# Optimization experiments

Measured on AMD Instinct MI355X. Metric: run time of the kernel, lower is better.

The kernel has to match this reference:

```python
import jax, jax.numpy as jnp
import numpy as np

B, C, H, W, K = 16, 256, 64, 64, 31
PAD = K // 2
EPS = 1e-5


def setup_inputs() -> dict:
    key = jax.random.key(0)
    k1, k2, k3 = jax.random.split(key, 3)
    x = jax.random.normal(k1, (B, C, H, W), dtype=jnp.float32)
    dw_w = jax.random.normal(k2, (C, 1, K, K), dtype=jnp.float32) * 0.02
    pw_w = jax.random.normal(k3, (C, C), dtype=jnp.float32) * 0.05
    gamma = jnp.ones((C,), dtype=jnp.float32)
    beta = jnp.zeros((C,), dtype=jnp.float32)
    return {"x": x, "dw_w": dw_w, "gamma": gamma, "beta": beta, "pw_w": pw_w}


def reference(x, dw_w, gamma, beta, pw_w):
    # depthwise 31x31 conv, padding=15, groups=C
    y = jax.lax.conv_general_dilated(
        x, dw_w,
        window_strides=(1, 1),
        padding=[(PAD, PAD), (PAD, PAD)],
        dimension_numbers=("NCHW", "OIHW", "NCHW"),
        feature_group_count=C,
    )
    # BatchNorm2d in training mode: biased batch stats over (N,H,W)
    mean = jnp.mean(y, axis=(0, 2, 3), keepdims=True)
    var = jnp.var(y, axis=(0, 2, 3), keepdims=True)  # biased, as torch uses for normalization
    g = gamma[None, :, None, None]
    b = beta[None, :, None, None]
    yn = (y - mean) * jax.lax.rsqrt(var + EPS) * g + b
    r = jax.nn.relu(yn)
    # pointwise 1x1 conv == channel-mixing matmul
    out = jnp.einsum("oc,bchw->bohw", pw_w, r)
    return out
```

## Files before the change

### kernel.cpp

```cpp
#include <hip/hip_runtime.h>
#include <hip/hip_bf16.h>

namespace {
constexpr int CB   = 256;
constexpr int HWp  = 4096;
constexpr int NB   = 16;

typedef __bf16    bf16x8 __attribute__((ext_vector_type(8)));
typedef float     f32x4  __attribute__((ext_vector_type(4)));
typedef float     f32x16 __attribute__((ext_vector_type(16)));
typedef _Float16  f16x2  __attribute__((ext_vector_type(2)));
typedef _Float16  f16x8  __attribute__((ext_vector_type(8)));

typedef __attribute__((address_space(1))) void gvoid;
typedef __attribute__((address_space(3))) void svoid;

__device__ __forceinline__ unsigned int pack2(float lo, float hi) {
#if __has_builtin(__builtin_amdgcn_cvt_pkrtz)
    return __builtin_bit_cast(unsigned int, __builtin_amdgcn_cvt_pkrtz(lo, hi));
#else
    f16x2 v; v[0] = (_Float16)lo; v[1] = (_Float16)hi;
    return __builtin_bit_cast(unsigned int, v);
#endif
}

constexpr int TOEP_PER_C = 31 * 4 * 64;
}

__global__ __launch_bounds__(256) void toep_kernel(
    const float* __restrict__ dw, uint4* __restrict__ toep)
{
    const int flat = blockIdx.x * 256 + threadIdx.x;
    const int lane = flat & 63;
    const int kq   = (flat >> 6) & 3;
    const int rc   = flat >> 8;
    const int r    = rc % 31;
    const int c    = rc / 31;
    const int i    = lane & 31;
    const int kbase = kq * 16 + (lane >> 5) * 8;

    const float* __restrict__ wr = dw + (size_t)c * 961 + r * 31;
    union { _Float16 h[8]; uint4 u; } out;
#pragma unroll
    for (int e = 0; e < 8; ++e) {
        const int t = kbase + e - i - 1;
        out.h[e] = (t >= 0 && t <= 30) ? (_Float16)wr[t] : (_Float16)0.f;
    }
    toep[flat] = out.u;
}

__global__ __launch_bounds__(256, 5) void dwconv_kernel(
    const float* __restrict__ x, const uint4* __restrict__ toep,
    float* __restrict__ y, float* __restrict__ gsum, float* __restrict__ gsumsq)
{
    __shared__ unsigned int xs[94 * 52];

    const int bc  = blockIdx.x;
    const int c   = bc & (CB - 1);
    const int tid = threadIdx.x;
    const float* __restrict__ xp = x + (size_t)bc * HWp;

    for (int idx = tid; idx < 1222; idx += 256)
        reinterpret_cast<uint4*>(xs)[idx] = uint4{0, 0, 0, 0};
    __syncthreads();
    {
        const int row = tid >> 2;
        const int q   = tid & 3;
        const float4* src = reinterpret_cast<const float4*>(xp + row * 64 + q * 16);
        float4 v0 = src[0], v1 = src[1], v2 = src[2], v3 = src[3];
        uint4 p0, p1;
        p0.x = pack2(v0.x, v0.y); p0.y = pack2(v0.z, v0.w);
        p0.z = pack2(v1.x, v1.y); p0.w = pack2(v1.z, v1.w);
        p1.x = pack2(v2.x, v2.y); p1.y = pack2(v2.z, v2.w);
        p1.z = pack2(v3.x, v3.y); p1.w = pack2(v3.z, v3.w);
        uint4* dst = reinterpret_cast<uint4*>(&xs[(row + 15) * 52 + 8 + q * 8]);
        dst[0] = p0; dst[1] = p1;
    }
    __syncthreads();

    const int lane = tid & 63;
    const int wid  = tid >> 6;
    const int h0   = wid * 16;
    const int j    = lane & 31;
    const int half = lane >> 5;

    const unsigned int* __restrict__ xb =
        &xs[(h0 + (j >> 1)) * 52 + (j & 1) * 16 + half * 4];
    const uint4* __restrict__ tp = toep + (size_t)c * TOEP_PER_C + lane;

    f32x16 acc = {};

    uint4 afA[4]; f16x8 bfA[4];
#pragma unroll
    for (int kq = 0; kq < 4; ++kq) {
        afA[kq] = tp[kq * 64];
        bfA[kq] = *reinterpret_cast<const f16x8*>(xb + kq * 8);
    }
#pragma unroll 2
    for (int r = 0; r < 31; ++r) {
        uint4 afB[4]; f16x8 bfB[4];
        if (r < 30) {
            const unsigned int* xr = xb + (r + 1) * 52;
#pragma unroll
            for (int kq = 0; kq < 4; ++kq) {
                afB[kq] = tp[((r + 1) * 4 + kq) * 64];
                bfB[kq] = *reinterpret_cast<const f16x8*>(xr + kq * 8);
            }
        }
#pragma unroll
        for (int kq = 0; kq < 4; ++kq)
            acc = __builtin_amdgcn_mfma_f32_32x32x16_f16(
                __builtin_bit_cast(f16x8, afA[kq]), bfA[kq], acc, 0, 0, 0);
#pragma unroll
        for (int kq = 0; kq < 4; ++kq) { afA[kq] = afB[kq]; bfA[kq] = bfB[kq]; }
    }

    const int hout = h0 + (j >> 1);
    float* __restrict__ yp = y + (size_t)bc * HWp + hout * 64 + (j & 1) * 32 + 4 * half;
#pragma unroll
    for (int g = 0; g < 4; ++g) {
        f32x4 v = { acc[4 * g + 0], acc[4 * g + 1], acc[4 * g + 2], acc[4 * g + 3] };
        *reinterpret_cast<f32x4*>(yp + 8 * g) = v;
    }

    float s = 0.f, s2 = 0.f;
#pragma unroll
    for (int t = 0; t < 16; ++t) { s += acc[t]; s2 = fmaf(acc[t], acc[t], s2); }
#pragma unroll
    for (int off = 32; off > 0; off >>= 1) {
        s  += __shfl_down(s,  off, 64);
        s2 += __shfl_down(s2, off, 64);
    }
    if (lane == 0) {
        atomicAdd(&gsum[c],   s);
        atomicAdd(&gsumsq[c], s2);
    }
}

__global__ __launch_bounds__(256) void pwb_kernel(
    const float* __restrict__ pw, __hip_bfloat16* __restrict__ pwb)
{
    const int idx = blockIdx.x * 256 + threadIdx.x;
    const float4 v = reinterpret_cast<const float4*>(pw)[idx];
    union { __hip_bfloat16 h[4]; uint2 u; } pk;
    pk.h[0] = __float2bfloat16(v.x); pk.h[1] = __float2bfloat16(v.y);
    pk.h[2] = __float2bfloat16(v.z); pk.h[3] = __float2bfloat16(v.w);
    reinterpret_cast<uint2*>(pwb)[idx] = pk.u;
}

__global__ __launch_bounds__(256) void stats_kernel(
    const float* __restrict__ gsum, const float* __restrict__ gsumsq,
    const float* __restrict__ gamma, const float* __restrict__ beta,
    float* __restrict__ scale, float* __restrict__ shift)
{
    const int tid = threadIdx.x;
    const float inv = 1.f / 65536.f;
    const float mean = gsum[tid] * inv;
    const float var  = gsumsq[tid] * inv - mean * mean;
    const float sc   = gamma[tid] * rsqrtf(var + 1e-5f);
    scale[tid] = sc;
    shift[tid] = beta[tid] - mean * sc;
}

__global__ __launch_bounds__(256) void normtrans_kernel(
    const float* __restrict__ y, const float* __restrict__ scale,
    const float* __restrict__ shift, __hip_bfloat16* __restrict__ rt)
{
    __shared__ __hip_bfloat16 tile[32][33];
    const int b   = blockIdx.z;
    const int c0  = blockIdx.y * 32;
    const int p0  = blockIdx.x * 32;
    const int tid = threadIdx.x;

    {
        const int cl  = tid >> 3;
        const int pl4 = (tid & 7) * 4;
        const float4 v = *reinterpret_cast<const float4*>(
            y + (size_t)(b * CB + c0 + cl) * HWp + p0 + pl4);
        const float sc = scale[c0 + cl], sh = shift[c0 + cl];
        tile[cl][pl4 + 0] = __float2bfloat16(fmaxf(fmaf(v.x, sc, sh), 0.f));
        tile[cl][pl4 + 1] = __float2bfloat16(fmaxf(fmaf(v.y, sc, sh), 0.f));
        tile[cl][pl4 + 2] = __float2bfloat16(fmaxf(fmaf(v.z, sc, sh), 0.f));
        tile[cl][pl4 + 3] = __float2bfloat16(fmaxf(fmaf(v.w, sc, sh), 0.f));
    }
    __syncthreads();
    {
        const int pl  = tid >> 3;
        const int cl4 = (tid & 7) * 4;
        union { __hip_bfloat16 h[4]; uint2 u; } pk;
#pragma unroll
        for (int k2 = 0; k2 < 4; ++k2) pk.h[k2] = tile[cl4 + k2][pl];
        *reinterpret_cast<uint2*>(
            rt + ((size_t)b * HWp + p0 + pl) * CB + c0 + cl4) = pk.u;
    }
}

__global__ __launch_bounds__(256, 2) void gemm_kernel(
    const __hip_bfloat16* __restrict__ pwb, const __hip_bfloat16* __restrict__ rt,
    float* __restrict__ out)
{
    __shared__ __hip_bfloat16 ldsA[128 * 32];
    __shared__ __hip_bfloat16 ldsB[128 * 32];

    const int tid  = threadIdx.x;
    const int lane = tid & 63;
    const int wid  = tid >> 6;
    const int b    = blockIdx.z;
    const int m0   = blockIdx.y * 128;
    const int p0   = blockIdx.x * 128;
    const int wm   = wid >> 1, wn = wid & 1;

    f32x4 acc[4][4];
#pragma unroll
    for (int mi = 0; mi < 4; ++mi)
#pragma unroll
        for (int ni = 0; ni < 4; ++ni) acc[mi][ni] = {0.f, 0.f, 0.f, 0.f};

    const int srow = lane >> 2;
    const int scol = (lane & 3) * 8;
    const int fr   = lane & 15;
    const int fk   = (lane >> 4) * 8;

    const size_t rtbase = (size_t)b * HWp;

    for (int ks = 0; ks < 8; ++ks) {
        const int k0 = ks * 32;
#pragma unroll
        for (int q = 0; q < 2; ++q) {
            const int issue = wid * 2 + q;
            const int row   = issue * 16 + srow;
            const __hip_bfloat16* gA = pwb + (size_t)(m0 + row) * CB + k0 + scol;
            const __hip_bfloat16* gB = rt + (rtbase + p0 + row) * CB + k0 + scol;
            __builtin_amdgcn_global_load_lds((gvoid*)gA, (svoid*)(ldsA + issue * 512), 16, 0, 0);
            __builtin_amdgcn_global_load_lds((gvoid*)gB, (svoid*)(ldsB + issue * 512), 16, 0, 0);
        }
        __syncthreads();

        bf16x8 af[4], bfr[4];
#pragma unroll
        for (int mi = 0; mi < 4; ++mi)
            af[mi] = *reinterpret_cast<const bf16x8*>(
                ldsA + (wm * 64 + mi * 16 + fr) * 32 + fk);
#pragma unroll
        for (int ni = 0; ni < 4; ++ni)
            bfr[ni] = *reinterpret_cast<const bf16x8*>(
                ldsB + (wn * 64 + ni * 16 + fr) * 32 + fk);

#pragma unroll
        for (int mi = 0; mi < 4; ++mi)
#pragma unroll
            for (int ni = 0; ni < 4; ++ni)
                acc[mi][ni] = __builtin_amdgcn_mfma_f32_16x16x32_bf16(
                    af[mi], bfr[ni], acc[mi][ni], 0, 0, 0);
        __syncthreads();
    }

    const int frow = (lane >> 4) * 4;
#pragma unroll
    for (int mi = 0; mi < 4; ++mi)
#pragma unroll
        for (int ni = 0; ni < 4; ++ni)
#pragma unroll
            for (int v = 0; v < 4; ++v) {
                const int o = m0 + wm * 64 + mi * 16 + frow + v;
                const int p = p0 + wn * 64 + ni * 16 + fr;
                out[((size_t)(b * CB + o)) * HWp + p] = acc[mi][ni][v];
            }
}

extern "C" void kernel_launch(void* const* d_in, const int* in_sizes, int n_in,
                              void* d_out, int out_size, void* d_ws, size_t ws_size,
                              hipStream_t stream) {
    (void)in_sizes; (void)n_in; (void)out_size; (void)ws_size;
    const float* x     = (const float*)d_in[0];
    const float* dw    = (const float*)d_in[1];
    const float* gamma = (const float*)d_in[2];
    const float* beta  = (const float*)d_in[3];
    const float* pw    = (const float*)d_in[4];
    float* out = (float*)d_out;

    char* ws = (char*)d_ws;
    uint4* toep        = (uint4*)ws;
    __hip_bfloat16* rt = (__hip_bfloat16*)ws;
    float* gsum   = (float*)(ws + (size_t)33554432);
    float* gsumsq = gsum + 256;
    float* scale  = gsum + 512;
    float* shift  = gsum + 768;
    __hip_bfloat16* pwb = (__hip_bfloat16*)(ws + (size_t)33554432 + 4096);

    hipMemsetAsync(gsum, 0, 2048, stream);

    pwb_kernel<<<dim3(64), 256, 0, stream>>>(pw, pwb);
    toep_kernel<<<dim3(7936), 256, 0, stream>>>(dw, toep);
    dwconv_kernel<<<dim3(NB * CB), 256, 0, stream>>>(x, toep, out, gsum, gsumsq);
    stats_kernel<<<dim3(1), 256, 0, stream>>>(gsum, gsumsq, gamma, beta, scale, shift);
    normtrans_kernel<<<dim3(128, 8, NB), 256, 0, stream>>>(out, scale, shift, rt);
    gemm_kernel<<<dim3(32, 2, NB), 256, 0, stream>>>(pwb, rt, out);
}
```

Before: 243.6 us.

## Process two images per dwconv block, store fp16 intermediate, fuse small prep kernels

The depthwise conv block now handles two batch images of the same channel, so each Toeplitz weight fragment loaded from global memory feeds twice as many MFMAs. The LDS halo gets an XOR swizzle with a 64-word row stride to avoid bank conflicts. The conv output is stored as fp16 instead of fp32, which halves the write and read traffic of the intermediate. The stats computation moves into the normalize/transpose kernel, which now uses wider 64-pixel tiles, and the pw/toeplitz prep kernels are merged into one launch. The trade-offs are extra precision loss in the stored intermediate and lower occupancy from the larger LDS footprint and launch bound.

```diff
diff --git a/kernel.cpp b/kernel.cpp
--- a/kernel.cpp
+++ b/kernel.cpp
@@ -25,12 +25,25 @@
 }
 
 constexpr int TOEP_PER_C = 31 * 4 * 64;
-}
-
-__global__ __launch_bounds__(256) void toep_kernel(
+constexpr int HALO_U32   = 94 * 64;
+}
+
+__global__ __launch_bounds__(256) void prep_kernel(
+    const float* __restrict__ pw, __hip_bfloat16* __restrict__ pwb,
     const float* __restrict__ dw, uint4* __restrict__ toep)
 {
-    const int flat = blockIdx.x * 256 + threadIdx.x;
+    const int bid = blockIdx.x;
+    const int tid = threadIdx.x;
+    if (bid < 64) {
+        const int idx = bid * 256 + tid;
+        const float4 v = reinterpret_cast<const float4*>(pw)[idx];
+        union { __hip_bfloat16 h[4]; uint2 u; } pk;
+        pk.h[0] = __float2bfloat16(v.x); pk.h[1] = __float2bfloat16(v.y);
+        pk.h[2] = __float2bfloat16(v.z); pk.h[3] = __float2bfloat16(v.w);
+        reinterpret_cast<uint2*>(pwb)[idx] = pk.u;
+        return;
+    }
+    const int flat = (bid - 64) * 256 + tid;
     const int lane = flat & 63;
     const int kq   = (flat >> 6) & 3;
     const int rc   = flat >> 8;
@@ -49,83 +62,108 @@
     toep[flat] = out.u;
 }
 
-__global__ __launch_bounds__(256, 5) void dwconv_kernel(
+__global__ __launch_bounds__(256, 3) void dwconv_kernel(
     const float* __restrict__ x, const uint4* __restrict__ toep,
-    float* __restrict__ y, float* __restrict__ gsum, float* __restrict__ gsumsq)
+    _Float16* __restrict__ y16, float* __restrict__ gsum, float* __restrict__ gsumsq)
 {
-    __shared__ unsigned int xs[94 * 52];
-
-    const int bc  = blockIdx.x;
-    const int c   = bc & (CB - 1);
+    __shared__ unsigned int xs[2 * HALO_U32];
+
+    const int bid = blockIdx.x;
+    const int c   = bid & 255;
+    const int bp  = bid >> 8;
     const int tid = threadIdx.x;
-    const float* __restrict__ xp = x + (size_t)bc * HWp;
-
-    for (int idx = tid; idx < 1222; idx += 256)
+
+    for (int idx = tid; idx < 2 * HALO_U32 / 4; idx += 256)
         reinterpret_cast<uint4*>(xs)[idx] = uint4{0, 0, 0, 0};
     __syncthreads();
+
     {
         const int row = tid >> 2;
         const int q   = tid & 3;
-        const float4* src = reinterpret_cast<const float4*>(xp + row * 64 + q * 16);
-        float4 v0 = src[0], v1 = src[1], v2 = src[2], v3 = src[3];
-        uint4 p0, p1;
-        p0.x = pack2(v0.x, v0.y); p0.y = pack2(v0.z, v0.w);
-        p0.z = pack2(v1.x, v1.y); p0.w = pack2(v1.z, v1.w);
-        p1.x = pack2(v2.x, v2.y); p1.y = pack2(v2.z, v2.w);
-        p1.z = pack2(v3.x, v3.y); p1.w = pack2(v3.z, v3.w);
-        uint4* dst = reinterpret_cast<uint4*>(&xs[(row + 15) * 52 + 8 + q * 8]);
-        dst[0] = p0; dst[1] = p1;
+        const int hr  = row + 15;
+        const int swz = (hr & 7) << 2;
+        const int p0  = (8  + q * 8) ^ swz;
+        const int p1  = (12 + q * 8) ^ swz;
+#pragma unroll
+        for (int img = 0; img < 2; ++img) {
+            const float4* src = reinterpret_cast<const float4*>(
+                x + ((size_t)((bp * 2 + img) * CB + c)) * HWp + row * 64 + q * 16);
+            float4 v0 = src[0], v1 = src[1], v2 = src[2], v3 = src[3];
+            uint4 a, b;
+            a.x = pack2(v0.x, v0.y); a.y = pack2(v0.z, v0.w);
+            a.z = pack2(v1.x, v1.y); a.w = pack2(v1.z, v1.w);
+            b.x = pack2(v2.x, v2.y); b.y = pack2(v2.z, v2.w);
+            b.z = pack2(v3.x, v3.y); b.w = pack2(v3.z, v3.w);
+            unsigned int* base = xs + img * HALO_U32 + hr * 64;
+            *reinterpret_cast<uint4*>(base + p0) = a;
+            *reinterpret_cast<uint4*>(base + p1) = b;
+        }
     }
     __syncthreads();
 
     const int lane = tid & 63;
     const int wid  = tid >> 6;
-    const int h0   = wid * 16;
     const int j    = lane & 31;
     const int half = lane >> 5;
-
-    const unsigned int* __restrict__ xb =
-        &xs[(h0 + (j >> 1)) * 52 + (j & 1) * 16 + half * 4];
+    const int rowb = wid * 16 + (j >> 1);
+    const int colb = (j & 1) * 16 + half * 4;
     const uint4* __restrict__ tp = toep + (size_t)c * TOEP_PER_C + lane;
 
-    f32x16 acc = {};
-
-    uint4 afA[4]; f16x8 bfA[4];
-#pragma unroll
-    for (int kq = 0; kq < 4; ++kq) {
-        afA[kq] = tp[kq * 64];
-        bfA[kq] = *reinterpret_cast<const f16x8*>(xb + kq * 8);
-    }
-#pragma unroll 2
+    f32x16 acc0 = {}, acc1 = {};
+    uint4 afA[4];
+#pragma unroll
+    for (int kq = 0; kq < 4; ++kq) afA[kq] = tp[kq * 64];
+
+#pragma unroll 1
     for (int r = 0; r < 31; ++r) {
-        uint4 afB[4]; f16x8 bfB[4];
+        uint4 afB[4];
         if (r < 30) {
-            const unsigned int* xr = xb + (r + 1) * 52;
-#pragma unroll
-            for (int kq = 0; kq < 4; ++kq) {
-                afB[kq] = tp[((r + 1) * 4 + kq) * 64];
-                bfB[kq] = *reinterpret_cast<const f16x8*>(xr + kq * 8);
-            }
+#pragma unroll
+            for (int kq = 0; kq < 4; ++kq) afB[kq] = tp[((r + 1) * 4 + kq) * 64];
+        }
+        const int row = rowb + r;
+        const int swz = (row & 7) << 2;
+        const unsigned int* __restrict__ xr = xs + row * 64;
+        f16x8 b0[4], b1[4];
+#pragma unroll
+        for (int kq = 0; kq < 4; ++kq) {
+            const int p = (colb + kq * 8) ^ swz;
+            b0[kq] = *reinterpret_cast<const f16x8*>(xr + p);
+            b1[kq] = *reinterpret_cast<const f16x8*>(xr + HALO_U32 + p);
         }
 #pragma unroll
         for (int kq = 0; kq < 4; ++kq)
-            acc = __builtin_amdgcn_mfma_f32_32x32x16_f16(
-                __builtin_bit_cast(f16x8, afA[kq]), bfA[kq], acc, 0, 0, 0);
-#pragma unroll
-        for (int kq = 0; kq < 4; ++kq) { afA[kq] = afB[kq]; bfA[kq] = bfB[kq]; }
-    }
-
-    const int hout = h0 + (j >> 1);
-    float* __restrict__ yp = y + (size_t)bc * HWp + hout * 64 + (j & 1) * 32 + 4 * half;
+            acc0 = __builtin_amdgcn_mfma_f32_32x32x16_f16(
+                __builtin_bit_cast(f16x8, afA[kq]), b0[kq], acc0, 0, 0, 0);
+#pragma unroll
+        for (int kq = 0; kq < 4; ++kq)
+            acc1 = __builtin_amdgcn_mfma_f32_32x32x16_f16(
+                __builtin_bit_cast(f16x8, afA[kq]), b1[kq], acc1, 0, 0, 0);
+        if (r < 30) {
+#pragma unroll
+            for (int kq = 0; kq < 4; ++kq) afA[kq] = afB[kq];
+        }
+    }
+
+    const size_t pl0 = ((size_t)(bp * 2 * CB + c)) * HWp + rowb * 64 + (j & 1) * 32 + 4 * half;
 #pragma unroll
     for (int g = 0; g < 4; ++g) {
-        f32x4 v = { acc[4 * g + 0], acc[4 * g + 1], acc[4 * g + 2], acc[4 * g + 3] };
-        *reinterpret_cast<f32x4*>(yp + 8 * g) = v;
+        uint2 u0, u1;
+        u0.x = pack2(acc0[4 * g + 0], acc0[4 * g + 1]);
+        u0.y = pack2(acc0[4 * g + 2], acc0[4 * g + 3]);
+        u1.x = pack2(acc1[4 * g + 0], acc1[4 * g + 1]);
+        u1.y = pack2(acc1[4 * g + 2], acc1[4 * g + 3]);
+        *reinterpret_cast<uint2*>(y16 + pl0 + 8 * g)            = u0;
+        *reinterpret_cast<uint2*>(y16 + pl0 + CB * HWp + 8 * g) = u1;
     }
 
     float s = 0.f, s2 = 0.f;
 #pragma unroll
-    for (int t = 0; t < 16; ++t) { s += acc[t]; s2 = fmaf(acc[t], acc[t], s2); }
+    for (int t = 0; t < 16; ++t) {
+        s += acc0[t] + acc1[t];
+        s2 = fmaf(acc0[t], acc0[t], s2);
+        s2 = fmaf(acc1[t], acc1[t], s2);
+    }
 #pragma unroll
     for (int off = 32; off > 0; off >>= 1) {
         s  += __shfl_down(s,  off, 64);
@@ -137,61 +175,51 @@
     }
 }
 
-__global__ __launch_bounds__(256) void pwb_kernel(
-    const float* __restrict__ pw, __hip_bfloat16* __restrict__ pwb)
-{
-    const int idx = blockIdx.x * 256 + threadIdx.x;
-    const float4 v = reinterpret_cast<const float4*>(pw)[idx];
-    union { __hip_bfloat16 h[4]; uint2 u; } pk;
-    pk.h[0] = __float2bfloat16(v.x); pk.h[1] = __float2bfloat16(v.y);
-    pk.h[2] = __float2bfloat16(v.z); pk.h[3] = __float2bfloat16(v.w);
-    reinterpret_cast<uint2*>(pwb)[idx] = pk.u;
-}
-
-__global__ __launch_bounds__(256) void stats_kernel(
+__global__ __launch_bounds__(256) void normtrans_kernel(
+    const _Float16* __restrict__ y16,
     const float* __restrict__ gsum, const float* __restrict__ gsumsq,
     const float* __restrict__ gamma, const float* __restrict__ beta,
-    float* __restrict__ scale, float* __restrict__ shift)
+    __hip_bfloat16* __restrict__ rt)
 {
-    const int tid = threadIdx.x;
-    const float inv = 1.f / 65536.f;
-    const float mean = gsum[tid] * inv;
-    const float var  = gsumsq[tid] * inv - mean * mean;
-    const float sc   = gamma[tid] * rsqrtf(var + 1e-5f);
-    scale[tid] = sc;
-    shift[tid] = beta[tid] - mean * sc;
-}
-
-__global__ __launch_bounds__(256) void normtrans_kernel(
-    const float* __restrict__ y, const float* __restrict__ scale,
-    const float* __restrict__ shift, __hip_bfloat16* __restrict__ rt)
-{
-    __shared__ __hip_bfloat16 tile[32][33];
+    __shared__ __hip_bfloat16 tile[32 * 72];
+    __shared__ float scsh[64];
     const int b   = blockIdx.z;
     const int c0  = blockIdx.y * 32;
-    const int p0  = blockIdx.x * 32;
+    const int p0  = blockIdx.x * 64;
     const int tid = threadIdx.x;
 
-    {
-        const int cl  = tid >> 3;
-        const int pl4 = (tid & 7) * 4;
-        const float4 v = *reinterpret_cast<const float4*>(
-            y + (size_t)(b * CB + c0 + cl) * HWp + p0 + pl4);
-        const float sc = scale[c0 + cl], sh = shift[c0 + cl];
-        tile[cl][pl4 + 0] = __float2bfloat16(fmaxf(fmaf(v.x, sc, sh), 0.f));
-        tile[cl][pl4 + 1] = __float2bfloat16(fmaxf(fmaf(v.y, sc, sh), 0.f));
-        tile[cl][pl4 + 2] = __float2bfloat16(fmaxf(fmaf(v.z, sc, sh), 0.f));
-        tile[cl][pl4 + 3] = __float2bfloat16(fmaxf(fmaf(v.w, sc, sh), 0.f));
+    const int cl  = tid >> 3;
+    const int pl8 = (tid & 7) * 8;
+    const uint4 raw = *reinterpret_cast<const uint4*>(
+        y16 + ((size_t)(b * CB + c0 + cl)) * HWp + p0 + pl8);
+    if (tid < 32) {
+        const int cc = c0 + tid;
+        const float inv = 1.f / 65536.f;
+        const float mean = gsum[cc] * inv;
+        const float var  = gsumsq[cc] * inv - mean * mean;
+        const float sc   = gamma[cc] * rsqrtf(var + 1e-5f);
+        scsh[tid]      = sc;
+        scsh[32 + tid] = beta[cc] - mean * sc;
     }
     __syncthreads();
     {
-        const int pl  = tid >> 3;
-        const int cl4 = (tid & 7) * 4;
-        union { __hip_bfloat16 h[4]; uint2 u; } pk;
-#pragma unroll
-        for (int k2 = 0; k2 < 4; ++k2) pk.h[k2] = tile[cl4 + k2][pl];
-        *reinterpret_cast<uint2*>(
-            rt + ((size_t)b * HWp + p0 + pl) * CB + c0 + cl4) = pk.u;
+        const float sc = scsh[cl], sh = scsh[32 + cl];
+        const f16x8 hv = __builtin_bit_cast(f16x8, raw);
+        union { __hip_bfloat16 h[8]; uint4 u; } o;
+#pragma unroll
+        for (int e = 0; e < 8; ++e)
+            o.h[e] = __float2bfloat16(fmaxf(fmaf((float)hv[e], sc, sh), 0.f));
+        *reinterpret_cast<uint4*>(&tile[cl * 72 + pl8]) = o.u;
+    }
+    __syncthreads();
+    {
+        const int pl  = tid >> 2;
+        const int cl8 = (tid & 3) * 8;
+        union { __hip_bfloat16 h[8]; uint4 u; } o;
+#pragma unroll
+        for (int e = 0; e < 8; ++e) o.h[e] = tile[(cl8 + e) * 72 + pl];
+        *reinterpret_cast<uint4*>(
+            rt + ((size_t)b * HWp + p0 + pl) * CB + c0 + cl8) = o.u;
     }
 }
 
@@ -284,16 +312,15 @@
     __hip_bfloat16* rt = (__hip_bfloat16*)ws;
     float* gsum   = (float*)(ws + (size_t)33554432);
     float* gsumsq = gsum + 256;
-    float* scale  = gsum + 512;
-    float* shift  = gsum + 768;
     __hip_bfloat16* pwb = (__hip_bfloat16*)(ws + (size_t)33554432 + 4096);
 
+    _Float16* y16 = (_Float16*)d_out;
+
     hipMemsetAsync(gsum, 0, 2048, stream);
 
-    pwb_kernel<<<dim3(64), 256, 0, stream>>>(pw, pwb);
-    toep_kernel<<<dim3(7936), 256, 0, stream>>>(dw, toep);
-    dwconv_kernel<<<dim3(NB * CB), 256, 0, stream>>>(x, toep, out, gsum, gsumsq);
-    stats_kernel<<<dim3(1), 256, 0, stream>>>(gsum, gsumsq, gamma, beta, scale, shift);
-    normtrans_kernel<<<dim3(128, 8, NB), 256, 0, stream>>>(out, scale, shift, rt);
+    prep_kernel<<<dim3(8000), 256, 0, stream>>>(pw, pwb, dw, toep);
+    dwconv_kernel<<<dim3(2048), 256, 0, stream>>>(x, toep, y16, gsum, gsumsq);
+    normtrans_kernel<<<dim3(64, 8, NB), 256, 0, stream>>>(y16, gsum, gsumsq,
+                                                          gamma, beta, rt);
     gemm_kernel<<<dim3(32, 2, NB), 256, 0, stream>>>(pwb, rt, out);
 }
```

Measured after the change: 219.8 us. 1.11x faster.
